# Performance work log

Measured on AMD Instinct MI355X. Metric: run time of the kernel, lower is better.

The kernel has to match this reference:

```python
import math
import jax, jax.numpy as jnp
import numpy as np

B, N, DIM, H, DH = 1, 2048, 1024, 16, 64
ROT = 32          # rotary dims (applied to first ROT dims of q/k/v)
MEM = 16          # num_mem_kv
NUM_BUCKETS, MAX_DIST = 32, 128
REL_SCALE = DH ** 0.5


def setup_inputs() -> dict:
    key = jax.random.key(0)
    ks = jax.random.split(key, 12)
    d = {}
    d['x'] = jax.random.normal(ks[0], (B, N, DIM), jnp.float32)
    d['rotary_pos_emb'] = jax.random.normal(ks[1], (1, 1, N, ROT), jnp.float32)
    s = 1.0 / math.sqrt(DIM)
    d['Wq'] = jax.random.normal(ks[2], (DIM, H * DH), jnp.float32) * s
    d['Wk'] = jax.random.normal(ks[3], (DIM, H * DH), jnp.float32) * s
    d['Wv'] = jax.random.normal(ks[4], (DIM, H * DH), jnp.float32) * s
    d['Wo'] = jax.random.normal(ks[5], (H * DH, DIM), jnp.float32) * (1.0 / math.sqrt(H * DH))
    d['bo'] = jnp.zeros((DIM,), jnp.float32)
    d['mem_k'] = jax.random.normal(ks[6], (H, MEM, DH), jnp.float32)
    d['mem_v'] = jax.random.normal(ks[7], (H, MEM, DH), jnp.float32)
    d['pre_proj'] = jax.random.normal(ks[8], (H, H), jnp.float32) * (1.0 / math.sqrt(H))
    d['post_proj'] = jax.random.normal(ks[9], (H, H), jnp.float32) * (1.0 / math.sqrt(H))
    d['qk_scale'] = jnp.full((1, H, 1, 1), -3.0, jnp.float32)
    d['rel_table'] = jax.random.normal(ks[10], (NUM_BUCKETS, H), jnp.float32) * 0.02
    return d


def _rotate_half(t):
    x1, x2 = jnp.split(t, 2, axis=-1)
    return jnp.concatenate([-x2, x1], axis=-1)


def _apply_rotary(t, freqs):
    # t: [b,h,n,ROT], freqs: [1,1,n,ROT]
    f = freqs[:, :, -t.shape[-2]:]
    return t * jnp.cos(f) + _rotate_half(t) * jnp.sin(f)


def _rel_bucket(n):
    # causal T5 bucket; n = q_pos - k_pos clamped to >= 0
    n = jnp.maximum(n, 0)
    max_exact = NUM_BUCKETS // 2
    is_small = n < max_exact
    nf = jnp.maximum(n, 1).astype(jnp.float32)
    val = max_exact + (jnp.log(nf / max_exact) / math.log(MAX_DIST / max_exact)
                       * (NUM_BUCKETS - max_exact)).astype(jnp.int32)
    val = jnp.minimum(val, NUM_BUCKETS - 1)
    return jnp.where(is_small, n, val)


def _l2norm(t, eps=1e-12):
    return t / jnp.maximum(jnp.linalg.norm(t, axis=-1, keepdims=True), eps)


def _forward(x, rotary_pos_emb, Wq, Wk, Wv, Wo, bo, mem_k, mem_v,
             pre_proj, post_proj, qk_scale, rel_table):
    b, n, _ = x.shape
    q = (x @ Wq).reshape(b, n, H, DH).transpose(0, 2, 1, 3)  # bhnd
    k = (x @ Wk).reshape(b, n, H, DH).transpose(0, 2, 1, 3)
    v = (x @ Wv).reshape(b, n, H, DH).transpose(0, 2, 1, 3)

    # rotary on first ROT dims of q, k AND v (faithful to source)
    def rot(t):
        return jnp.concatenate([_apply_rotary(t[..., :ROT], rotary_pos_emb), t[..., ROT:]], axis=-1)
    q, k, v = rot(q), rot(k), rot(v)

    # prepend learned memory kv
    mk = jnp.broadcast_to(mem_k[None], (b, H, MEM, DH))
    mv = jnp.broadcast_to(mem_v[None], (b, H, MEM, DH))
    k = jnp.concatenate([mk, k], axis=-2)  # [b,h,j,d], j = n + MEM
    v = jnp.concatenate([mv, v], axis=-2)

    # qk-norm with learned per-head scale
    q, k = _l2norm(q), _l2norm(k)
    scale = 1.0 / jnp.clip(jnp.exp(qk_scale), 0.01, None)  # [1,h,1,1]

    dots = jnp.einsum('bhid,bhjd->bhij', q, k) * scale

    # talking heads (pre-softmax)
    dots = jnp.einsum('bhij,hk->bkij', dots, pre_proj)

    # relative position bias (T5 buckets)
    i, j = dots.shape[-2], dots.shape[-1]
    q_pos = jnp.arange(i)
    k_pos = jnp.arange(j)
    rp = _rel_bucket(q_pos[:, None] - k_pos[None, :])     # [i,j]
    bias = rel_table[rp]                                   # [i,j,h]
    dots = dots + jnp.transpose(bias, (2, 0, 1))[None] * REL_SCALE

    # causal mask, left-padded False over the MEM columns
    mask_value = -jnp.finfo(dots.dtype).max
    r = jnp.arange(i)
    causal = r[:, None] < r[None, :]                       # [i,i]
    causal = jnp.concatenate([jnp.zeros((i, j - i), bool), causal], axis=1)
    dots = jnp.where(causal[None, None], mask_value, dots)

    attn = jax.nn.softmax(dots, axis=-1)
    # talking heads (post-softmax)
    attn = jnp.einsum('bhij,hk->bkij', attn, post_proj)

    out = jnp.einsum('bhij,bhjd->bhid', attn, v)
    out = out.transpose(0, 2, 1, 3).reshape(b, n, H * DH)
    return out @ Wo + bo


def reference(x, rotary_pos_emb, Wq, Wk, Wv, Wo, bo, mem_k, mem_v,
              pre_proj, post_proj, qk_scale, rel_table):
    return _forward(x, rotary_pos_emb, Wq, Wk, Wv, Wo, bo, mem_k, mem_v,
                    pre_proj, post_proj, qk_scale, rel_table)
```

## Files before the change

kernel.cpp:

```cpp
#include <hip/hip_runtime.h>
#include <math.h>
#include <float.h>

#define N_SEQ 2048
#define DIMN  1024
#define NH    16
#define DH    64
#define ROT   32
#define MEM   16
#define JTOT  (N_SEQ + MEM)
#define JP    2112
#define NB    32
#define REL_SCALE 8.0f
#define C_SPLIT 6
#define JSP   352
#define SST   20

typedef __attribute__((ext_vector_type(8))) _Float16 half8;
typedef __attribute__((ext_vector_type(4))) _Float16 half4;
typedef __attribute__((ext_vector_type(4))) float floatx4;

__global__ __launch_bounds__(256) void convert_f16(
    const float* __restrict__ in, _Float16* __restrict__ out, int n4)
{
  const int t = blockIdx.x * 256 + threadIdx.x;
  if (t >= n4) return;
  float4 v = ((const float4*)in)[t];
  half4 o = { (_Float16)v.x, (_Float16)v.y, (_Float16)v.z, (_Float16)v.w };
  *(half4*)&out[(size_t)t * 4] = o;
}

__global__ __launch_bounds__(256) void convtrans(
    const float* __restrict__ W, _Float16* __restrict__ WT, int K, int N)
{
  __shared__ _Float16 tile[64][72];
  const int k0 = blockIdx.y * 64, n0 = blockIdx.x * 64;
  const int t = threadIdx.x;
#pragma unroll
  for (int p = 0; p < 4; ++p) {
    const int r = (t >> 4) + 16 * p;
    const int c = (t & 15) * 4;
    float4 wv = *(const float4*)&W[(size_t)(k0 + r) * N + n0 + c];
    tile[r][c + 0] = (_Float16)wv.x;
    tile[r][c + 1] = (_Float16)wv.y;
    tile[r][c + 2] = (_Float16)wv.z;
    tile[r][c + 3] = (_Float16)wv.w;
  }
  __syncthreads();
#pragma unroll
  for (int p = 0; p < 2; ++p) {
    const int n = (t >> 3) + 32 * p;
    const int kc = (t & 7) * 8;
    half8 o;
#pragma unroll
    for (int j = 0; j < 8; ++j) o[j] = tile[kc + j][n];
    *(half8*)&WT[(size_t)(n0 + n) * K + k0 + kc] = o;
  }
}

__global__ __launch_bounds__(256) void gemm_f16(
    const _Float16* __restrict__ A, const _Float16* __restrict__ BT,
    float* __restrict__ C, const float* __restrict__ bias,
    int M, int K, int N)
{
  const int tid = threadIdx.x;
  const int w = tid >> 6, lane = tid & 63;
  const int m0 = blockIdx.y * 64 + w * 16;
  const int n0 = blockIdx.x * 64;
  const int lr = lane & 15, lk = (lane >> 4) * 8;
  const _Float16* Ap = A + (size_t)(m0 + lr) * K + lk;
  const _Float16* Bp = BT + (size_t)(n0 + lr) * K + lk;
  floatx4 acc[4];
#pragma unroll
  for (int T = 0; T < 4; ++T) acc[T] = (floatx4){0.f, 0.f, 0.f, 0.f};
#pragma unroll 2
  for (int k0 = 0; k0 < K; k0 += 32) {
    half8 af = *(const half8*)(Ap + k0);
#pragma unroll
    for (int T = 0; T < 4; ++T) {
      half8 bf = *(const half8*)(Bp + (size_t)T * 16 * K + k0);
      acc[T] = __builtin_amdgcn_mfma_f32_16x16x32_f16(af, bf, acc[T], 0, 0, 0);
    }
  }
#pragma unroll
  for (int T = 0; T < 4; ++T) {
    const int col = n0 + T * 16 + lr;
    const float bb = bias ? bias[col] : 0.f;
#pragma unroll
    for (int r = 0; r < 4; ++r) {
      const int row = m0 + (lane >> 4) * 4 + r;
      C[(size_t)row * N + col] = acc[T][r] + bb;
    }
  }
}

__global__ __launch_bounds__(256) void postproc(
    const float* __restrict__ tmp, const float* __restrict__ rot,
    const float* __restrict__ mem_k, const float* __restrict__ mem_v,
    const float* __restrict__ qk_scale,
    _Float16* __restrict__ qh, _Float16* __restrict__ kh, _Float16* __restrict__ vh)
{
  const int gw = (blockIdx.x * 256 + threadIdx.x) >> 6;
  const int lane = threadIdx.x & 63;
  const int TQ = NH * N_SEQ;
  const int TM = TQ + NH * MEM;
  const int TP = TM + NH * (JP - JTOT);
  if (gw < TQ) {
    const int h = gw >> 11;
    const int i = gw & (N_SEQ - 1);
    const size_t base = (size_t)i * DIMN + h * DH + lane;
    float q = tmp[base];
    float k = tmp[base + (size_t)N_SEQ * DIMN];
    float v = tmp[base + 2 * (size_t)N_SEQ * DIMN];
    float cf = 1.f, sf = 0.f;
    if (lane < ROT) { float f = rot[(size_t)i * ROT + lane]; cf = cosf(f); sf = sinf(f); }
    float qp = __shfl_xor(q, 16);
    float kp = __shfl_xor(k, 16);
    float vp = __shfl_xor(v, 16);
    if (lane < ROT) {
      float sgn = (lane < 16) ? -1.f : 1.f;
      q = q * cf + sgn * qp * sf;
      k = k * cf + sgn * kp * sf;
      v = v * cf + sgn * vp * sf;
    }
    float nq = q * q, nk = k * k;
#pragma unroll
    for (int off = 32; off; off >>= 1) { nq += __shfl_xor(nq, off); nk += __shfl_xor(nk, off); }
    q *= 1.f / fmaxf(sqrtf(nq), 1e-12f);
    k *= 1.f / fmaxf(sqrtf(nk), 1e-12f);
    float scl = 1.0f / fmaxf(__expf(qk_scale[h]), 0.01f);
    qh[((size_t)h * N_SEQ + i) * DH + lane] = (_Float16)(q * scl);
    kh[((size_t)h * JP + MEM + i) * DH + lane] = (_Float16)k;
    vh[((size_t)h * JP + MEM + i) * DH + lane] = (_Float16)v;
  } else if (gw < TM) {
    const int r = gw - TQ;
    const int h = r >> 4, mm = r & 15;
    float k = mem_k[((size_t)h * MEM + mm) * DH + lane];
    float v = mem_v[((size_t)h * MEM + mm) * DH + lane];
    float nk = k * k;
#pragma unroll
    for (int off = 32; off; off >>= 1) nk += __shfl_xor(nk, off);
    k *= 1.f / fmaxf(sqrtf(nk), 1e-12f);
    kh[((size_t)h * JP + mm) * DH + lane] = (_Float16)k;
    vh[((size_t)h * JP + mm) * DH + lane] = (_Float16)v;
  } else if (gw < TP) {
    const int r = gw - TM;
    const int h = r / (JP - JTOT), jr = JTOT + r % (JP - JTOT);
    kh[((size_t)h * JP + jr) * DH + lane] = (_Float16)0.f;
    vh[((size_t)h * JP + jr) * DH + lane] = (_Float16)0.f;
  }
}

__global__ __launch_bounds__(256) void transpose_v(
    const _Float16* __restrict__ vh, _Float16* __restrict__ vT)
{
  __shared__ _Float16 tile[64][72];
  const int h = blockIdx.y;
  const int j0 = blockIdx.x * 64;
  const int t = threadIdx.x;
#pragma unroll
  for (int p = 0; p < 2; ++p) {
    const int jr = (t >> 3) + 32 * p;
    const int dc = (t & 7) * 8;
    half8 v = *(const half8*)(vh + ((size_t)h * JP + j0 + jr) * DH + dc);
    *(half8*)&tile[jr][dc] = v;
  }
  __syncthreads();
#pragma unroll
  for (int p = 0; p < 2; ++p) {
    const int d = (t >> 3) + 32 * p;
    const int jc = (t & 7) * 8;
    half8 o;
#pragma unroll
    for (int r = 0; r < 8; ++r) o[r] = tile[jc + r][d];
    *(half8*)(vT + ((size_t)h * DH + d) * JP + j0 + jc) = o;
  }
}

__device__ __forceinline__ int rel_bucket(int n) {
  if (n < 0) n = 0;
  if (n < 16) return n;
  int v = 16 + (int)(logf((float)n * 0.0625f) * 7.6944042f);
  return v > 31 ? 31 : v;
}

__global__ __launch_bounds__(512, 2) void attn_pass1(
    const _Float16* __restrict__ qh, const _Float16* __restrict__ kh,
    const float* __restrict__ pre_proj, const float* __restrict__ rel_table,
    float* __restrict__ mpart, float* __restrict__ lpart)
{
  const int i0 = blockIdx.x * 16;
  const int c = blockIdx.y;
  const int jlo = c * JSP;
  if (jlo >= i0 + 32) return;
  const int jhi = min(min(jlo + JSP, JP), (i0 + 63) & ~31);
  const int tid = threadIdx.x;
  const int lane = tid & 63, w = tid >> 6;
  const int n15 = lane & 15, q4 = lane >> 4;

  __shared__ _Float16 S16[512 * SST];
  __shared__ float relt_f[NB * NH];

  relt_f[tid] = rel_table[tid] * REL_SCALE;

  half4 preA;
#pragma unroll
  for (int t = 0; t < 4; ++t) preA[t] = (_Float16)pre_proj[(q4 * 4 + t) * 16 + n15];

  half8 qf[2][2];
#pragma unroll
  for (int n = 0; n < 2; ++n) {
    const int h = w * 2 + n;
    const _Float16* qb = qh + ((size_t)h * N_SEQ + i0 + n15) * DH + q4 * 8;
    qf[n][0] = *(const half8*)qb;
    qf[n][1] = *(const half8*)(qb + 32);
  }
  float m2[2][4], l2[2][4];
#pragma unroll
  for (int p = 0; p < 2; ++p)
#pragma unroll
    for (int r = 0; r < 4; ++r) { m2[p][r] = -1e30f; l2[p][r] = 0.f; }
  __syncthreads();

  for (int jb = jlo; jb < jhi; jb += 32) {
#pragma unroll
    for (int n = 0; n < 2; ++n) {
      const int h = w * 2 + n;
#pragma unroll
      for (int T = 0; T < 2; ++T) {
        floatx4 acc = {0.f, 0.f, 0.f, 0.f};
        const _Float16* kb = kh + ((size_t)h * JP + jb + 16 * T + n15) * DH + q4 * 8;
        acc = __builtin_amdgcn_mfma_f32_16x16x32_f16(qf[n][0], *(const half8*)kb, acc, 0, 0, 0);
        acc = __builtin_amdgcn_mfma_f32_16x16x32_f16(qf[n][1], *(const half8*)(kb + 32), acc, 0, 0, 0);
        const int jcol = n15 + 16 * T;
#pragma unroll
        for (int r = 0; r < 4; ++r) {
          const int i = q4 * 4 + r;
          S16[(i * 32 + jcol) * SST + h] = (_Float16)acc[r];
        }
      }
    }
    __syncthreads();
#pragma unroll
    for (int mm = 0; mm < 4; ++mm) {
      const int mc = w * 4 + mm;
      const int par = mm >> 1;
      const int i = 2 * w + par;
      const int col = mc * 16 + n15;
      half4 bf = *(const half4*)&S16[col * SST + q4 * 4];
      floatx4 sp = __builtin_amdgcn_mfma_f32_16x16x16f16(preA, bf, (floatx4){0.f, 0.f, 0.f, 0.f}, 0, 0, 0);
      const int ig = i0 + i;
      const int jg = jb + n15 + (mc & 1) * 16;
      const bool valid = (jg <= ig + MEM) && (jg < JTOT);
      if (valid) {
        const int rb = rel_bucket(ig - jg);
        float4 rr = *(const float4*)&relt_f[rb * 16 + q4 * 4];
        const float rv[4] = { rr.x, rr.y, rr.z, rr.w };
#pragma unroll
        for (int r = 0; r < 4; ++r) {
          const float s = sp[r] + rv[r];
          const float mo = m2[par][r];
          const float mn = fmaxf(mo, s);
          const float e = __expf(fminf(mo, s) - mn);
          l2[par][r] = (s > mo) ? (l2[par][r] * e + 1.0f) : (l2[par][r] + e);
          m2[par][r] = mn;
        }
      }
    }
    __syncthreads();
  }
#pragma unroll
  for (int off = 1; off < 16; off <<= 1) {
#pragma unroll
    for (int p = 0; p < 2; ++p)
#pragma unroll
      for (int r = 0; r < 4; ++r) {
        float mo = __shfl_xor(m2[p][r], off);
        float lo = __shfl_xor(l2[p][r], off);
        float mn = fmaxf(m2[p][r], mo);
        l2[p][r] = l2[p][r] * __expf(m2[p][r] - mn) + lo * __expf(mo - mn);
        m2[p][r] = mn;
      }
  }
  if (n15 == 0) {
#pragma unroll
    for (int p = 0; p < 2; ++p) {
      const int ig = i0 + 2 * w + p;
#pragma unroll
      for (int r = 0; r < 4; ++r) {
        const int k = q4 * 4 + r;
        mpart[((size_t)c * NH + k) * N_SEQ + ig] = m2[p][r];
        lpart[((size_t)c * NH + k) * N_SEQ + ig] = l2[p][r];
      }
    }
  }
}

__global__ __launch_bounds__(256) void merge_ml(
    const float* __restrict__ mpart, const float* __restrict__ lpart,
    float* __restrict__ Mf, float* __restrict__ Lf)
{
  const int t = blockIdx.x * 256 + threadIdx.x;
  const int i = t & (N_SEQ - 1);
  const int lim = (i & ~15) + 32;
  const int h = t >> 11;
  float m = -1e30f;
#pragma unroll
  for (int c = 0; c < C_SPLIT; ++c)
    if (c * JSP < lim) m = fmaxf(m, mpart[((size_t)c * NH + h) * N_SEQ + i]);
  float l = 0.f;
#pragma unroll
  for (int c = 0; c < C_SPLIT; ++c)
    if (c * JSP < lim) {
      float mc = mpart[((size_t)c * NH + h) * N_SEQ + i];
      l += lpart[((size_t)c * NH + h) * N_SEQ + i] * __expf(mc - m);
    }
  Mf[t] = m;
  Lf[t] = l;
}

__global__ __launch_bounds__(512, 2) void attn_pass2(
    const _Float16* __restrict__ qh, const _Float16* __restrict__ kh,
    const _Float16* __restrict__ vT,
    const float* __restrict__ pre_proj, const float* __restrict__ post_proj,
    const float* __restrict__ rel_table,
    const float* __restrict__ Mf, const float* __restrict__ Lf,
    float* __restrict__ ctx)
{
  const int i0 = blockIdx.x * 16;
  const int c = blockIdx.y;
  const int jlo = c * JSP;
  if (jlo >= i0 + 32) return;
  const int jhi = min(min(jlo + JSP, JP), (i0 + 63) & ~31);
  const int tid = threadIdx.x;
  const int lane = tid & 63, w = tid >> 6;
  const int n15 = lane & 15, q4 = lane >> 4;

  __shared__ _Float16 S16[512 * SST];
  __shared__ _Float16 P2[256 * 40];
  __shared__ float relt_f[NB * NH];
  __shared__ float Ml4[256], iLl4[256];

  relt_f[tid] = rel_table[tid] * REL_SCALE;
  if (tid < 256) {
    const int i = tid >> 4, k = tid & 15;
    Ml4[tid] = Mf[(size_t)k * N_SEQ + i0 + i];
    iLl4[tid] = 1.0f / Lf[(size_t)k * N_SEQ + i0 + i];
  }

  half4 preA, postA;
#pragma unroll
  for (int t = 0; t < 4; ++t) {
    preA[t] = (_Float16)pre_proj[(q4 * 4 + t) * 16 + n15];
    postA[t] = (_Float16)post_proj[(q4 * 4 + t) * 16 + n15];
  }

  half8 qf[2][2];
#pragma unroll
  for (int n = 0; n < 2; ++n) {
    const int h = w * 2 + n;
    const _Float16* qb = qh + ((size_t)h * N_SEQ + i0 + n15) * DH + q4 * 8;
    qf[n][0] = *(const half8*)qb;
    qf[n][1] = *(const half8*)(qb + 32);
  }
  floatx4 oacc[2][4];
#pragma unroll
  for (int n = 0; n < 2; ++n)
#pragma unroll
    for (int T = 0; T < 4; ++T) oacc[n][T] = (floatx4){0.f, 0.f, 0.f, 0.f};
  __syncthreads();

  for (int jb = jlo; jb < jhi; jb += 32) {
#pragma unroll
    for (int n = 0; n < 2; ++n) {
      const int h = w * 2 + n;
#pragma unroll
      for (int T = 0; T < 2; ++T) {
        floatx4 acc = {0.f, 0.f, 0.f, 0.f};
        const _Float16* kb = kh + ((size_t)h * JP + jb + 16 * T + n15) * DH + q4 * 8;
        acc = __builtin_amdgcn_mfma_f32_16x16x32_f16(qf[n][0], *(const half8*)kb, acc, 0, 0, 0);
        acc = __builtin_amdgcn_mfma_f32_16x16x32_f16(qf[n][1], *(const half8*)(kb + 32), acc, 0, 0, 0);
        const int jcol = n15 + 16 * T;
#pragma unroll
        for (int r = 0; r < 4; ++r) {
          const int i = q4 * 4 + r;
          S16[(i * 32 + jcol) * SST + h] = (_Float16)acc[r];
        }
      }
    }
    __syncthreads();
#pragma unroll
    for (int mm = 0; mm < 4; ++mm) {
      const int mc = w * 4 + mm;
      const int i = 2 * w + (mm >> 1);
      const int jj = n15 + (mc & 1) * 16;
      const int col = mc * 16 + n15;
      half4 bf = *(const half4*)&S16[col * SST + q4 * 4];
      floatx4 sp = __builtin_amdgcn_mfma_f32_16x16x16f16(preA, bf, (floatx4){0.f, 0.f, 0.f, 0.f}, 0, 0, 0);
      const int ig = i0 + i;
      const int jg = jb + jj;
      const bool valid = (jg <= ig + MEM) && (jg < JTOT);
      const int rb = rel_bucket(ig - jg);
      float4 rr = *(const float4*)&relt_f[rb * 16 + q4 * 4];
      float4 Mr = *(const float4*)&Ml4[i * 16 + q4 * 4];
      float4 Lr = *(const float4*)&iLl4[i * 16 + q4 * 4];
      const float rv[4] = { rr.x, rr.y, rr.z, rr.w };
      const float Mv[4] = { Mr.x, Mr.y, Mr.z, Mr.w };
      const float Lv[4] = { Lr.x, Lr.y, Lr.z, Lr.w };
      half4 p4;
#pragma unroll
      for (int r = 0; r < 4; ++r) {
        const float p = valid ? __expf(sp[r] + rv[r] - Mv[r]) * Lv[r] : 0.f;
        p4[r] = (_Float16)p;
      }
      floatx4 od = __builtin_amdgcn_mfma_f32_16x16x16f16(postA, p4, (floatx4){0.f, 0.f, 0.f, 0.f}, 0, 0, 0);
#pragma unroll
      for (int r = 0; r < 4; ++r) {
        const int k2 = q4 * 4 + r;
        P2[(k2 * 16 + i) * 40 + jj] = (_Float16)od[r];
      }
    }
    __syncthreads();
#pragma unroll
    for (int n = 0; n < 2; ++n) {
      const int h = w * 2 + n;
      half8 af = *(const half8*)&P2[(h * 16 + n15) * 40 + q4 * 8];
#pragma unroll
      for (int T = 0; T < 4; ++T) {
        const _Float16* vb = vT + ((size_t)h * DH + 16 * T + n15) * JP + jb + q4 * 8;
        oacc[n][T] = __builtin_amdgcn_mfma_f32_16x16x32_f16(af, *(const half8*)vb, oacc[n][T], 0, 0, 0);
      }
    }
  }
#pragma unroll
  for (int n = 0; n < 2; ++n) {
    const int h = w * 2 + n;
#pragma unroll
    for (int T = 0; T < 4; ++T)
#pragma unroll
      for (int r = 0; r < 4; ++r) {
        const int row = i0 + q4 * 4 + r;
        const int col = h * DH + 16 * T + n15;
        atomicAdd(&ctx[(size_t)row * DIMN + col], oacc[n][T][r]);
      }
  }
}

extern "C" void kernel_launch(void* const* d_in, const int* in_sizes, int n_in,
                              void* d_out, int out_size, void* d_ws, size_t ws_size,
                              hipStream_t stream)
{
  const float* x         = (const float*)d_in[0];
  const float* rot       = (const float*)d_in[1];
  const float* Wq        = (const float*)d_in[2];
  const float* Wk        = (const float*)d_in[3];
  const float* Wv        = (const float*)d_in[4];
  const float* Wo        = (const float*)d_in[5];
  const float* bo        = (const float*)d_in[6];
  const float* mem_k     = (const float*)d_in[7];
  const float* mem_v     = (const float*)d_in[8];
  const float* pre_proj  = (const float*)d_in[9];
  const float* post_proj = (const float*)d_in[10];
  const float* qk_scale  = (const float*)d_in[11];
  const float* rel_table = (const float*)d_in[12];
  float* out = (float*)d_out;
  float* ws  = (float*)d_ws;

  float* tmp    = ws;
  float* ctx    = ws;
  float* mpart  = ws + 6291456;
  float* lpart  = mpart + 196608;
  float* Mf     = lpart + 196608;
  float* Lf     = Mf + 32768;
  _Float16* xh  = (_Float16*)(Lf + 32768);
  _Float16* WqT = xh + 2097152;
  _Float16* WkT = WqT + 1048576;
  _Float16* WvT = WkT + 1048576;
  _Float16* WoT = WvT + 1048576;
  _Float16* qh  = WoT + 1048576;
  _Float16* kh  = qh + 2097152;
  _Float16* vT  = kh + 2162688;
  _Float16* vh  = vT + 2162688;
  _Float16* ctxh = xh;
  (void)in_sizes; (void)n_in; (void)out_size; (void)ws_size;

  convert_f16<<<2048, 256, 0, stream>>>(x, xh, N_SEQ * DIMN / 4);
  convtrans<<<dim3(16, 16), 256, 0, stream>>>(Wq, WqT, DIMN, DIMN);
  convtrans<<<dim3(16, 16), 256, 0, stream>>>(Wk, WkT, DIMN, DIMN);
  convtrans<<<dim3(16, 16), 256, 0, stream>>>(Wv, WvT, DIMN, DIMN);
  convtrans<<<dim3(16, 16), 256, 0, stream>>>(Wo, WoT, DIMN, DIMN);

  dim3 gB(DIMN / 64, N_SEQ / 64);
  gemm_f16<<<gB, 256, 0, stream>>>(xh, WqT, tmp, nullptr, N_SEQ, DIMN, DIMN);
  gemm_f16<<<gB, 256, 0, stream>>>(xh, WkT, tmp + (size_t)N_SEQ * DIMN, nullptr, N_SEQ, DIMN, DIMN);
  gemm_f16<<<gB, 256, 0, stream>>>(xh, WvT, tmp + 2 * (size_t)N_SEQ * DIMN, nullptr, N_SEQ, DIMN, DIMN);

  {
    const int waves = NH * N_SEQ + NH * MEM + NH * (JP - JTOT);
    postproc<<<waves / 4, 256, 0, stream>>>(tmp, rot, mem_k, mem_v, qk_scale, qh, kh, vh);
  }
  transpose_v<<<dim3(JP / 64, NH), 256, 0, stream>>>(vh, vT);

  hipMemsetAsync(ctx, 0, (size_t)N_SEQ * DIMN * sizeof(float), stream);

  attn_pass1<<<dim3(N_SEQ / 16, C_SPLIT), 512, 0, stream>>>(
      qh, kh, pre_proj, rel_table, mpart, lpart);
  merge_ml<<<NH * N_SEQ / 256, 256, 0, stream>>>(mpart, lpart, Mf, Lf);
  attn_pass2<<<dim3(N_SEQ / 16, C_SPLIT), 512, 0, stream>>>(
      qh, kh, vT, pre_proj, post_proj, rel_table, Mf, Lf, ctx);

  convert_f16<<<2048, 256, 0, stream>>>(ctx, ctxh, N_SEQ * DIMN / 4);
  gemm_f16<<<gB, 256, 0, stream>>>(ctxh, WoT, out, bo, N_SEQ, DIMN, DIMN);
}
```

Baseline: 476.5 us.

## Fuse QKV projections into one GEMM and pack pass2 LDS tables into padding

Replaces the three separate Q/K/V projection GEMMs with one GEMM over the concatenated transposed weights (WqT, WkT and WvT sit next to each other in the workspace), writing an interleaved [N,3072] output that postproc now reads with a stride of 3072. It also moves pass2's rel-bias, row-max and inverse-sum tables into the unused padding columns of the P2 shared buffer, cutting that kernel's LDS footprint to allow more resident blocks. This saves two kernel launches and gives the projection a larger grid. The cost is reliance on the weight buffers being contiguous, and on the padding columns not being overwritten by the P2 writes.

Result: faster. 455.2 us (-4.5%).

```diff
diff --git a/kernel.cpp b/kernel.cpp
--- a/kernel.cpp
+++ b/kernel.cpp
@@ -108,10 +108,10 @@
   if (gw < TQ) {
     const int h = gw >> 11;
     const int i = gw & (N_SEQ - 1);
-    const size_t base = (size_t)i * DIMN + h * DH + lane;
+    const size_t base = (size_t)i * 3072 + h * DH + lane;
     float q = tmp[base];
-    float k = tmp[base + (size_t)N_SEQ * DIMN];
-    float v = tmp[base + 2 * (size_t)N_SEQ * DIMN];
+    float k = tmp[base + 1024];
+    float v = tmp[base + 2048];
     float cf = 1.f, sf = 0.f;
     if (lane < ROT) { float f = rot[(size_t)i * ROT + lane]; cf = cosf(f); sf = sinf(f); }
     float qp = __shfl_xor(q, 16);
@@ -338,15 +338,14 @@
 
   __shared__ _Float16 S16[512 * SST];
   __shared__ _Float16 P2[256 * 40];
-  __shared__ float relt_f[NB * NH];
-  __shared__ float Ml4[256], iLl4[256];
-
-  relt_f[tid] = rel_table[tid] * REL_SCALE;
+
+#define HOLE(rr) ((float*)&P2[(rr) * 40 + 32])
   if (tid < 256) {
     const int i = tid >> 4, k = tid & 15;
-    Ml4[tid] = Mf[(size_t)k * N_SEQ + i0 + i];
-    iLl4[tid] = 1.0f / Lf[(size_t)k * N_SEQ + i0 + i];
-  }
+    HOLE(tid >> 2)[tid & 3] = Mf[(size_t)k * N_SEQ + i0 + i];
+    HOLE((tid >> 2) + 64)[tid & 3] = 1.0f / Lf[(size_t)k * N_SEQ + i0 + i];
+  }
+  HOLE((tid >> 2) + 128)[tid & 3] = rel_table[tid] * REL_SCALE;
 
   half4 preA, postA;
 #pragma unroll
@@ -401,9 +400,9 @@
       const int jg = jb + jj;
       const bool valid = (jg <= ig + MEM) && (jg < JTOT);
       const int rb = rel_bucket(ig - jg);
-      float4 rr = *(const float4*)&relt_f[rb * 16 + q4 * 4];
-      float4 Mr = *(const float4*)&Ml4[i * 16 + q4 * 4];
-      float4 Lr = *(const float4*)&iLl4[i * 16 + q4 * 4];
+      float4 rr = *(const float4*)HOLE(128 + rb * 4 + q4);
+      float4 Mr = *(const float4*)HOLE(i * 4 + q4);
+      float4 Lr = *(const float4*)HOLE(64 + i * 4 + q4);
       const float rv[4] = { rr.x, rr.y, rr.z, rr.w };
       const float Mv[4] = { Mr.x, Mr.y, Mr.z, Mr.w };
       const float Lv[4] = { Lr.x, Lr.y, Lr.z, Lr.w };
@@ -432,6 +431,7 @@
       }
     }
   }
+#undef HOLE
 #pragma unroll
   for (int n = 0; n < 2; ++n) {
     const int h = w * 2 + n;
@@ -490,10 +490,8 @@
   convtrans<<<dim3(16, 16), 256, 0, stream>>>(Wv, WvT, DIMN, DIMN);
   convtrans<<<dim3(16, 16), 256, 0, stream>>>(Wo, WoT, DIMN, DIMN);
 
-  dim3 gB(DIMN / 64, N_SEQ / 64);
-  gemm_f16<<<gB, 256, 0, stream>>>(xh, WqT, tmp, nullptr, N_SEQ, DIMN, DIMN);
-  gemm_f16<<<gB, 256, 0, stream>>>(xh, WkT, tmp + (size_t)N_SEQ * DIMN, nullptr, N_SEQ, DIMN, DIMN);
-  gemm_f16<<<gB, 256, 0, stream>>>(xh, WvT, tmp + 2 * (size_t)N_SEQ * DIMN, nullptr, N_SEQ, DIMN, DIMN);
+  gemm_f16<<<dim3(3072 / 64, N_SEQ / 64), 256, 0, stream>>>(
+      xh, WqT, tmp, nullptr, N_SEQ, DIMN, 3072);
 
   {
     const int waves = NH * N_SEQ + NH * MEM + NH * (JP - JTOT);
@@ -510,5 +508,6 @@
       qh, kh, vT, pre_proj, post_proj, rel_table, Mf, Lf, ctx);
 
   convert_f16<<<2048, 256, 0, stream>>>(ctx, ctxh, N_SEQ * DIMN / 4);
-  gemm_f16<<<gB, 256, 0, stream>>>(ctxh, WoT, out, bo, N_SEQ, DIMN, DIMN);
-}
+  gemm_f16<<<dim3(DIMN / 64, N_SEQ / 64), 256, 0, stream>>>(
+      ctxh, WoT, out, bo, N_SEQ, DIMN, DIMN);
+}
```
